# Performance work log

Measured on AMD Instinct MI355X. Metric: run time of the kernel, lower is better.

## Reference

```python
import jax, jax.numpy as jnp
import numpy as np

STRIDE = 16
SIZES = np.array([128.0, 256.0, 512.0], np.float32)
RATIOS = np.array([0.5, 1.0, 2.0], np.float32)
N_POS, N_NEG = 32, 32          # n_sample=64, pos_ratio=0.5
POS_THR, NEG_THR = 0.7, 0.2
W_CONF, W_REG = 1.0, 5.0


def _conv(x, w, b, stride, pad):
    y = jax.lax.conv_general_dilated(x, w, (stride, stride), [(pad, pad), (pad, pad)],
                                     dimension_numbers=('NCHW', 'OIHW', 'NCHW'))
    return y + b[None, :, None, None]


def _anchors(fw, fh, stride):
    # 9 anchors per center: 3 sizes x 3 aspect ratios
    ws = (SIZES[:, None] * np.sqrt(RATIOS)[None, :]).reshape(-1)
    hs = (SIZES[:, None] / np.sqrt(RATIOS)[None, :]).reshape(-1)
    wh = jnp.asarray(np.stack([ws, hs], -1))                      # (9,2)
    cx = (jnp.arange(fw, dtype=jnp.float32) + 0.5) * stride
    cy = (jnp.arange(fh, dtype=jnp.float32) + 0.5) * stride
    gx, gy = jnp.meshgrid(cx, cy, indexing='ij')                  # x-major, like the torch list comp
    ctr = jnp.stack([gx, gy], -1)[:, :, None, :]                  # (fw,fh,1,2)
    tl = ctr - wh / 2.0
    xywh = jnp.concatenate([tl, jnp.broadcast_to(wh, tl.shape)], -1)  # (fw,fh,9,4)
    return xywh.reshape(-1, 4)


def _xywh_to_xyxy(b):
    return jnp.concatenate([b[:, :2], b[:, :2] + b[:, 2:]], -1)


def _iou(a, b):  # a [N,4], b [M,4], xyxy
    lt = jnp.maximum(a[:, None, :2], b[None, :, :2])
    rb = jnp.minimum(a[:, None, 2:], b[None, :, 2:])
    inter = jnp.clip(rb - lt, 0.0).prod(-1)
    aa = (a[:, 2] - a[:, 0]) * (a[:, 3] - a[:, 1])
    ab = (b[:, 2] - b[:, 0]) * (b[:, 3] - b[:, 1])
    return inter / (aa[:, None] + ab[None, :] - inter)


def _head_flat(y, per):  # [1, 9*per, H, W] -> [W*H*9, per], matching anchor flatten order
    _, _, H, W = y.shape
    return y[0].reshape(9, per, H, W).transpose(3, 2, 0, 1).reshape(-1, per)


def _apply_offsets(boxes, off):  # decode proposals from xyxy boxes + (dx,dy,dw,dh)
    w = boxes[:, 2] - boxes[:, 0]; h = boxes[:, 3] - boxes[:, 1]
    cx = boxes[:, 0] + 0.5 * w;    cy = boxes[:, 1] + 0.5 * h
    ncx = cx + off[:, 0] * w;      ncy = cy + off[:, 1] * h
    nw = w * jnp.exp(off[:, 2]);   nh = h * jnp.exp(off[:, 3])
    return jnp.stack([ncx - nw / 2, ncy - nh / 2, ncx + nw / 2, ncy + nh / 2], -1)


def _box_offset(anc, gt):
    aw = anc[:, 2] - anc[:, 0]; ah = anc[:, 3] - anc[:, 1]
    acx = anc[:, 0] + 0.5 * aw; acy = anc[:, 1] + 0.5 * ah
    gw = gt[:, 2] - gt[:, 0];   gh = gt[:, 3] - gt[:, 1]
    gcx = gt[:, 0] + 0.5 * gw;  gcy = gt[:, 1] + 0.5 * gh
    return jnp.stack([(gcx - acx) / aw, (gcy - acy) / ah,
                      jnp.log(gw / aw), jnp.log(gh / ah)], -1)


def setup_inputs():
    key = jax.random.key(0)
    ks = jax.random.split(key, 12)
    img_data = jax.random.normal(ks[0], (1, 3, 1600, 1600), jnp.float32)
    x1 = jax.random.uniform(ks[1], (64,), minval=0.0, maxval=1400.0)
    y1 = jax.random.uniform(ks[2], (64,), minval=0.0, maxval=1400.0)
    bw = jax.random.uniform(ks[3], (64,), minval=32.0, maxval=200.0)
    bh = jax.random.uniform(ks[4], (64,), minval=32.0, maxval=200.0)
    gt_boxes = jnp.stack([x1, y1, x1 + bw, y1 + bh], -1)[None]   # [1,64,4], all valid (no -1 pad)
    gt_classes = jax.random.randint(ks[5], (1, 64), 1, 21, jnp.int32)
    def w(k, shape, fan):
        return jax.random.normal(k, shape, jnp.float32) * np.float32(np.sqrt(2.0 / fan))
    return dict(
        img_data=img_data, gt_boxes=gt_boxes, gt_classes=gt_classes,
        w1=w(ks[6], (64, 3, 7, 7), 3 * 49),      b1=jnp.zeros(64, jnp.float32),
        w2=w(ks[7], (256, 64, 3, 3), 64 * 9),    b2=jnp.zeros(256, jnp.float32),
        w_rpn=w(ks[8], (256, 256, 3, 3), 256 * 9), b_rpn=jnp.zeros(256, jnp.float32),
        w_cls=w(ks[9], (18, 256, 1, 1), 256),    b_cls=jnp.zeros(18, jnp.float32),
        w_reg=w(ks[10], (36, 256, 1, 1), 256),   b_reg=jnp.zeros(36, jnp.float32),
    )


def reference(img_data, gt_boxes, gt_classes, w1, b1, w2, b2, w_rpn, b_rpn, w_cls, b_cls, w_reg, b_reg):
    # --- feature extractor (total stride 16) ---
    fm = jax.nn.relu(_conv(img_data, w1, b1, 4, 3))
    fm = jax.nn.relu(_conv(fm, w2, b2, 4, 1))            # [1,256,100,100]
    H, W = fm.shape[2], fm.shape[3]
    # --- anchors + IoU matching ---
    anchors_xywh = _anchors(W, H, STRIDE)                # [N,4] xywh
    anchors_xyxy = _xywh_to_xyxy(anchors_xywh)
    gt = gt_boxes[0]                                     # [M,4], all valid
    ious = _iou(anchors_xyxy, gt)                        # [N,M]
    N = ious.shape[0]
    gt_max = ious.max(0)                                 # best iou per gt
    is_gt_best = (ious == gt_max[None, :]).any(1)        # torch: where(iou == gt_max)[0]
    anc_argmax = ious.argmax(1)
    anc_max = ious.max(1)
    labels = jnp.full((N,), -1.0, jnp.float32)
    labels = jnp.where(anc_max < NEG_THR, 0.0, labels)
    labels = jnp.where(is_gt_best, 1.0, labels)
    labels = jnp.where(anc_max > POS_THR, 1.0, labels)
    # --- deterministic pos/neg sampling (fixed sizes; replaces randperm subsampling) ---
    idx = jnp.arange(N, dtype=jnp.float32)
    _, pos_index = jax.lax.top_k(jnp.where(labels == 1.0, anc_max, -1.0), N_POS)
    _, neg_index = jax.lax.top_k(jnp.where(labels == 0.0, 1e6 - idx, -1e9), N_NEG)
    bboxes_pos = anchors_xyxy[pos_index]                 # box_convert(xywh->xyxy) of pos anchors
    # --- proposal module (RPN head) ---
    h = jax.nn.relu(_conv(fm, w_rpn, b_rpn, 1, 1))
    cls = _head_flat(_conv(h, w_cls, b_cls, 1, 0), 2)    # [N,2]
    reg = _head_flat(_conv(h, w_reg, b_reg, 1, 0), 4)    # [N,4]
    pos_score = cls[pos_index]
    neg_score = cls[neg_index]
    offset_pos = reg[pos_index]
    proposals = _apply_offsets(bboxes_pos, offset_pos)
    # --- losses ---
    gt_offset = _box_offset(bboxes_pos, gt[anc_argmax[pos_index]])
    logits = jnp.concatenate([pos_score, neg_score], 0)  # [64,2]
    tgt = jnp.concatenate([jnp.ones(N_POS, jnp.int32), jnp.zeros(N_NEG, jnp.int32)])
    logp = jax.nn.log_softmax(logits, -1)
    cls_loss = -logp[jnp.arange(N_POS + N_NEG), tgt].mean()
    d = gt_offset - offset_pos
    ad = jnp.abs(d)
    reg_loss = jnp.where(ad < 1.0, 0.5 * d * d, ad - 0.5).mean()
    total_rpn_loss = W_CONF * cls_loss + W_REG * reg_loss
    gt_cls_pos = gt_classes[0][anc_argmax[pos_index]]
    return (total_rpn_loss, fm, proposals, pos_index, gt_cls_pos)
```

## Files before the change

kernel.cpp:

```cpp
#include <hip/hip_runtime.h>
#include <math.h>


#define CAP 4096

typedef __attribute__((ext_vector_type(8))) short bf16x8;
typedef __attribute__((ext_vector_type(4))) float f32x4;

#define OFF_F1T     0
#define OFF_HBUF    0
#define OFF_FMT     5171328
#define OFF_CPART   6503040
#define OFF_RPART   7223040
#define OFF_WA1     8663040
#define OFF_W9_2    8672448
#define OFF_W9_3    8746176
#define OFF_WTC     9041088
#define OFF_WTG     9045696
#define OFF_AARG    9054912
#define OFF_NEGM    9144912
#define OFF_POSM    9147728
#define OFF_GTMAX   9150544
#define OFF_PIDX    9150624
#define OFF_NIDX    9150656
#define OFF_CANDS   9150688
#define OFF_CANDI   9154784

__device__ __forceinline__ unsigned short f2bf(float f) {
    unsigned int u = __float_as_uint(f);
    u += 0x7fffu + ((u >> 16) & 1u);
    return (unsigned short)(u >> 16);
}

__device__ __forceinline__ void anchor_box(int i, float& x0, float& y0,
                                           float& x1, float& y1, float& area) {
#pragma clang fp contract(off)
    const float sizes[3]  = {128.f, 256.f, 512.f};
    const float ratios[3] = {0.5f, 1.f, 2.f};
    int a = i % 9;
    int q = i / 9;
    int iy = q % 100;
    int ix = q / 100;
    int s = a / 3, r = a % 3;
    float sq = sqrtf(ratios[r]);
    float w = sizes[s] * sq;
    float h = sizes[s] / sq;
    float cx = ((float)ix + 0.5f) * 16.0f;
    float cy = ((float)iy + 0.5f) * 16.0f;
    x0 = cx - w * 0.5f;
    y0 = cy - h * 0.5f;
    x1 = x0 + w;
    y1 = y0 + h;
    area = (x1 - x0) * (y1 - y0);
}

__device__ __forceinline__ float iou_one(float ax0, float ay0, float ax1, float ay1, float aa,
                                         float bx0, float by0, float bx1, float by1, float ab) {
#pragma clang fp contract(off)
    float ltx = fmaxf(ax0, bx0), lty = fmaxf(ay0, by0);
    float rbx = fminf(ax1, bx1), rby = fminf(ay1, by1);
    float iw = fmaxf(rbx - ltx, 0.0f);
    float ih = fmaxf(rby - lty, 0.0f);
    float inter = iw * ih;
    return inter / ((aa + ab) - inter);
}

__global__ __launch_bounds__(256) void setup_kernel(const float* __restrict__ wc, float* __restrict__ wtc,
                                                    const float* __restrict__ wg, float* __restrict__ wtg,
                                                    const float* __restrict__ w1, unsigned short* __restrict__ wa1,
                                                    const float* __restrict__ w2, unsigned short* __restrict__ w9_2,
                                                    const float* __restrict__ wr, unsigned short* __restrict__ w9_3,
                                                    unsigned int* __restrict__ f1t_u, unsigned int* __restrict__ fmt_u,
                                                    unsigned int* __restrict__ gtmax) {
    int i = blockIdx.x * 256 + threadIdx.x;
    if (i < 65) { gtmax[i] = 0u; return; }
    i -= 65;
    if (i < 103040) {
        if (i < 51328) {
            int p = i >> 5, part = i & 31;
            int x, y;
            if (p < 804) { y = (p < 402) ? 0 : 401; x = p % 402; }
            else { int j = p - 804; x = (j < 400) ? 0 : 401; y = 1 + (j % 400); }
            f1t_u[(y * 402 + x) * 32 + part] = 0u;
        } else {
            int i2 = i - 51328;
            int p = i2 >> 7, part = i2 & 127;
            int x, y;
            if (p < 204) { y = (p < 102) ? 0 : 101; x = p % 102; }
            else { int j = p - 204; x = (j < 100) ? 0 : 101; y = 1 + (j % 100); }
            fmt_u[(y * 102 + x) * 128 + part] = 0u;
        }
        return;
    }
    i -= 103040;
    if (i < 4608) { int c = i / 256, k = i - c * 256; wtc[k * 18 + c] = wc[i]; return; }
    i -= 4608;
    if (i < 9216) { int c = i / 256, k = i - c * 256; wtg[k * 36 + c] = wg[i]; return; }
    i -= 9216;
    if (i < 10240) {
        int oc = i / 160, k = i - oc * 160;
        wa1[i] = (k < 147) ? f2bf(w1[oc * 147 + k]) : (unsigned short)0;
        return;
    }
    i -= 10240;
    if (i < 147456) {
        int kk = i / 16384; int rem = i - kk * 16384;
        int oc = rem / 64, ic = rem - oc * 64;
        w9_2[i] = f2bf(w2[(oc * 64 + ic) * 9 + kk]);
        return;
    }
    i -= 147456;
    if (i < 589824) {
        int cc = i / 16384; int rem = i - cc * 16384;
        int oc = rem / 64, icl = rem - oc * 64;
        int kk = cc / 4, ch = cc - kk * 4;
        w9_3[i] = f2bf(wr[(oc * 256 + ch * 64 + icl) * 9 + kk]);
    }
}

__global__ __launch_bounds__(256) void conv1_mfma(const float* __restrict__ img,
                                                  const unsigned short* __restrict__ wA,
                                                  const float* __restrict__ bias,
                                                  unsigned short* __restrict__ f1t) {
    __shared__ float sin_[3 * 7 * 260];
    __shared__ unsigned short tileT[64 * 72];
    int t = threadIdx.x;
    int wave = t >> 6, lane = t & 63;
    int quad = lane >> 4, l16 = lane & 15;
    int oy = blockIdx.y;
    int ox0 = blockIdx.x * 64;
    int gx0 = ox0 * 4 - 3;
    int gy0 = 4 * oy - 3;
    for (int idx = t; idx < 3 * 7 * 259; idx += 256) {
        int ic = idx / (7 * 259);
        int r = idx - ic * 7 * 259;
        int ky = r / 259, c = r - ky * 259;
        int gy = gy0 + ky, gx = gx0 + c;
        float v = 0.f;
        if (gy >= 0 && gy < 1600 && gx >= 0 && gx < 1600)
            v = img[(ic * 1600 + gy) * 1600 + gx];
        sin_[(ic * 7 + ky) * 260 + c] = v;
    }
    bf16x8 afr[5];
    {
        const bf16x8* ap = (const bf16x8*)(wA + (wave * 16 + l16) * 160 + quad * 8);
#pragma unroll
        for (int c = 0; c < 5; c++) afr[c] = ap[c * 4];
    }
    __syncthreads();

    f32x4 acc[4];
#pragma unroll
    for (int j = 0; j < 4; j++) acc[j] = (f32x4){0.f, 0.f, 0.f, 0.f};
    int q8 = quad * 8;
    int col4[4];
#pragma unroll
    for (int j = 0; j < 4; j++) col4[j] = 4 * (j * 16 + l16);

#pragma unroll
    for (int ch = 0; ch < 5; ch++) {
        float val[4][8];
#pragma unroll
        for (int jj = 0; jj < 8; jj++) {
            int k = ch * 32 + q8 + jj;
            int ic = (k * 335) >> 14;
            int r = k - ic * 49;
            int ky = (r * 37) >> 8;
            int kx = r - ky * 7;
            bool valid = (k < 147);
            int base = valid ? ((ic * 7 + ky) * 260 + kx) : 0;
#pragma unroll
            for (int j = 0; j < 4; j++) {
                float v = sin_[base + col4[j]];
                val[j][jj] = valid ? v : 0.f;
            }
        }
#pragma unroll
        for (int j = 0; j < 4; j++) {
            bf16x8 b;
#pragma unroll
            for (int jj = 0; jj < 8; jj++) b[jj] = (short)f2bf(val[j][jj]);
            acc[j] = __builtin_amdgcn_mfma_f32_16x16x32_bf16(afr[ch], b, acc[j], 0, 0, 0);
        }
    }
#pragma unroll
    for (int reg = 0; reg < 4; reg++) {
        int oc = wave * 16 + quad * 4 + reg;
        float bv = bias[oc];
#pragma unroll
        for (int j = 0; j < 4; j++) {
            int px = j * 16 + l16;
            tileT[px * 72 + oc] = f2bf(fmaxf(acc[j][reg] + bv, 0.f));
        }
    }
    __syncthreads();
    int px = t >> 2, part = t & 3;
    int ox = ox0 + px;
    if (ox < 400) {
        int row = (oy + 1) * 402 + ox + 1;
        uint4 v = *(const uint4*)(tileT + px * 72 + part * 16);
        *(uint4*)(f1t + row * 64 + part * 16) = v;
    }
}

template<int ICC, int RS, int S, bool WRT>
__global__ __launch_bounds__(256, 2) void conv_gemm(const unsigned short* __restrict__ Bt,
                                                    const unsigned short* __restrict__ A9,
                                                    const float* __restrict__ bias,
                                                    float* __restrict__ outF,
                                                    unsigned short* __restrict__ outT) {
    const int NC = ICC / 64;
    const int HC = S * 24 + 3;
    const int LROW = ICC + 8;
    __shared__ unsigned short blds[3 * HC * LROW];
    __shared__ unsigned short alds[256 * 72];
    int t = threadIdx.x;
    int xs = blockIdx.x, y = blockIdx.y;

    const int CHW = ICC / 8;
    for (int idx = t; idx < 3 * HC * CHW; idx += 256) {
        int row = idx / CHW, e = idx - row * CHW;
        int ky = row / HC, c = row - ky * HC;
        const uint4* src = (const uint4*)(Bt + ((size_t)(S * y + ky) * RS + S * xs * 25 + c) * ICC) + e;
        *(uint4*)(blds + row * LROW + e * 8) = *src;
    }
    int wave = t >> 6, lane = t & 63;
    int quad = lane >> 4, l16 = lane & 15;
    int oc0 = wave * 64;
    int pxe0 = min(l16, 24);
    int pxe1 = min(16 + l16, 24);

    f32x4 acc[4][2];
#pragma unroll
    for (int mt = 0; mt < 4; mt++)
#pragma unroll
        for (int j = 0; j < 2; j++) acc[mt][j] = (f32x4){0.f, 0.f, 0.f, 0.f};

    const unsigned short* a0 = alds + (oc0 + l16) * 72 + quad * 8;
    for (int cc = 0; cc < 9 * NC; cc++) {
        int pass = cc / NC, ch = cc - pass * NC;
        int ky = pass / 3, kx = pass - (pass / 3) * 3;
        __syncthreads();
        const uint4* asrc = (const uint4*)(A9 + (size_t)cc * 16384);
#pragma unroll
        for (int i = 0; i < 8; i++) {
            int e = i * 256 + t;
            *(uint4*)(alds + (e >> 3) * 72 + (e & 7) * 8) = asrc[e];
        }
        __syncthreads();
        const unsigned short* b0 = blds + (ky * HC + S * pxe0 + kx) * LROW + ch * 64 + quad * 8;
        const unsigned short* b1 = blds + (ky * HC + S * pxe1 + kx) * LROW + ch * 64 + quad * 8;
#pragma unroll
        for (int kcl = 0; kcl < 2; kcl++) {
            bf16x8 bf0 = *(const bf16x8*)(b0 + kcl * 32);
            bf16x8 bf1 = *(const bf16x8*)(b1 + kcl * 32);
#pragma unroll
            for (int mt = 0; mt < 4; mt++) {
                bf16x8 af = *(const bf16x8*)(a0 + mt * 16 * 72 + kcl * 32);
                acc[mt][0] = __builtin_amdgcn_mfma_f32_16x16x32_bf16(af, bf0, acc[mt][0], 0, 0, 0);
                acc[mt][1] = __builtin_amdgcn_mfma_f32_16x16x32_bf16(af, bf1, acc[mt][1], 0, 0, 0);
            }
        }
    }
#pragma unroll
    for (int mt = 0; mt < 4; mt++) {
#pragma unroll
        for (int reg = 0; reg < 4; reg++) {
            int oc = oc0 + mt * 16 + quad * 4 + reg;
            float bv = bias[oc];
#pragma unroll
            for (int j = 0; j < 2; j++) {
                int pl = j * 16 + l16;
                if (pl < 25) {
                    int p = y * 100 + xs * 25 + pl;
                    float v = fmaxf(acc[mt][j][reg] + bv, 0.f);
                    outF[oc * 10000 + p] = v;
                    if (WRT) {
                        int r = (y + 1) * 102 + xs * 25 + pl + 1;
                        outT[r * 256 + oc] = f2bf(v);
                    }
                }
            }
        }
    }
}

__global__ __launch_bounds__(64) void head_kernel(const float* __restrict__ hbuf,
                                                  const float* __restrict__ wtc,
                                                  const float* __restrict__ wtg,
                                                  float* __restrict__ cpart,
                                                  float* __restrict__ rpart) {
    int p = blockIdx.x * 64 + threadIdx.x;
    int ch = blockIdx.y;
    int ic0 = ch * 64;
    if (p >= 10000) return;
    float acc[54];
#pragma unroll
    for (int j = 0; j < 54; j++) acc[j] = 0.f;
    for (int ic = 0; ic < 64; ic++) {
        float v = hbuf[(ic0 + ic) * 10000 + p];
        const float* wc_ = wtc + (ic0 + ic) * 18;
#pragma unroll
        for (int j = 0; j < 18; j++) acc[j] += v * wc_[j];
        const float* wg_ = wtg + (ic0 + ic) * 36;
#pragma unroll
        for (int j = 0; j < 36; j++) acc[18 + j] += v * wg_[j];
    }
    for (int j = 0; j < 18; j++) cpart[(ch * 18 + j) * 10000 + p] = acc[j];
    for (int j = 0; j < 36; j++) rpart[(ch * 36 + j) * 10000 + p] = acc[18 + j];
}

__global__ __launch_bounds__(256) void iou_pass1(const float* __restrict__ gt,
                                                 int* __restrict__ aarg,
                                                 unsigned int* __restrict__ gtmax) {
    __shared__ float sg[64][4];
    __shared__ float sarea[64];
    __shared__ unsigned int smax[64];
    int t = threadIdx.x;
    if (t < 64) {
#pragma clang fp contract(off)
        float b0 = gt[t * 4 + 0], b1 = gt[t * 4 + 1];
        float b2 = gt[t * 4 + 2], b3 = gt[t * 4 + 3];
        sg[t][0] = b0; sg[t][1] = b1; sg[t][2] = b2; sg[t][3] = b3;
        sarea[t] = (b2 - b0) * (b3 - b1);
        smax[t] = 0u;
    }
    __syncthreads();
    int i = blockIdx.x * 256 + t;
    int iq = min(i, 89999);
    float x0, y0, x1, y1, aa;
    anchor_box(iq, x0, y0, x1, y1, aa);
    float best = -1.f;
    int bestj = 0;
    for (int j = 0; j < 64; j++) {
        float v = iou_one(x0, y0, x1, y1, aa, sg[j][0], sg[j][1], sg[j][2], sg[j][3], sarea[j]);
        if (v > best) { best = v; bestj = j; }
        float vm = v;
#pragma unroll
        for (int off = 32; off > 0; off >>= 1) vm = fmaxf(vm, __shfl_xor(vm, off));
        if ((t & 63) == 0) atomicMax(&smax[j], __float_as_uint(vm));
    }
    if (i < 90000) aarg[i] = bestj;
    __syncthreads();
    if (t < 64) atomicMax(&gtmax[t], smax[t]);
}

__global__ __launch_bounds__(256) void iou_pass2(const float* __restrict__ gt,
                                                 const unsigned int* __restrict__ gtmax,
                                                 unsigned long long* __restrict__ negmask,
                                                 unsigned long long* __restrict__ posmask,
                                                 float* __restrict__ cand_s,
                                                 int* __restrict__ cand_i,
                                                 unsigned int* __restrict__ cnt) {
    __shared__ float sg[64][4];
    __shared__ float sarea[64];
    __shared__ float sgm[64];
    int t = threadIdx.x;
    if (t < 64) {
#pragma clang fp contract(off)
        float b0 = gt[t * 4 + 0], b1 = gt[t * 4 + 1];
        float b2 = gt[t * 4 + 2], b3 = gt[t * 4 + 3];
        sg[t][0] = b0; sg[t][1] = b1; sg[t][2] = b2; sg[t][3] = b3;
        sarea[t] = (b2 - b0) * (b3 - b1);
        sgm[t] = __uint_as_float(gtmax[t]);
    }
    __syncthreads();
    int i = blockIdx.x * 256 + t;
    if (i >= 90000) return;
    float x0, y0, x1, y1, aa;
    anchor_box(i, x0, y0, x1, y1, aa);
    float best = -1.f;
    bool isbest = false;
    for (int j = 0; j < 64; j++) {
        float v = iou_one(x0, y0, x1, y1, aa, sg[j][0], sg[j][1], sg[j][2], sg[j][3], sarea[j]);
        if (v > best) best = v;
        if (v == sgm[j]) isbest = true;
    }
    float label = -1.f;
    if (best < 0.2f) label = 0.f;
    if (isbest) label = 1.f;
    if (best > 0.7f) label = 1.f;
    unsigned long long negb = __ballot(label == 0.f);
    unsigned long long posb = __ballot(label == 1.f);
    if ((t & 63) == 0) { negmask[i >> 6] = negb; posmask[i >> 6] = posb; }
    if (label == 1.f) {
        unsigned int p = atomicAdd(cnt, 1u);
        if (p < CAP) { cand_s[p] = best; cand_i[p] = i; }
    }
}

__device__ int first32_from_mask(const unsigned long long* __restrict__ mask,
                                 bool invert, int* __restrict__ outIdx,
                                 int* scnt, int t) {
    const int NW = 1407;
    const int WPT = 6;
    unsigned long long mw[WPT];
    int cnt = 0;
#pragma unroll
    for (int u = 0; u < WPT; u++) {
        int w = t * WPT + u;
        unsigned long long m = 0ull;
        if (w < NW) {
            m = mask[w];
            if (invert) m = ~m;
            if (w == NW - 1) m &= 0xFFFFull;
        }
        mw[u] = m;
        cnt += __builtin_popcountll(m);
    }
    scnt[t] = cnt;
    __syncthreads();
    for (int off = 1; off < 256; off <<= 1) {
        int v = (t >= off) ? scnt[t - off] : 0;
        __syncthreads();
        scnt[t] += v;
        __syncthreads();
    }
    int total = scnt[255];
    int pref = scnt[t] - cnt;
    if (pref < 32) {
#pragma unroll
        for (int u = 0; u < WPT; u++) {
            unsigned long long m = mw[u];
            int wbase = (t * WPT + u) * 64;
            while (m && pref < 32) {
                int b = __builtin_ctzll(m);
                outIdx[pref++] = wbase + b;
                m &= m - 1;
            }
        }
    }
    __syncthreads();
    return total;
}

__global__ __launch_bounds__(256) void select_kernel(const unsigned long long* __restrict__ negmask,
                                                     const unsigned long long* __restrict__ posmask,
                                                     const float* __restrict__ cand_s,
                                                     const int* __restrict__ cand_i,
                                                     const unsigned int* __restrict__ cnt,
                                                     int* __restrict__ pidx,
                                                     int* __restrict__ nidx) {
    __shared__ float cs[CAP + 32];
    __shared__ int ci[CAP + 32];
    __shared__ int scnt[256];
    __shared__ int sfill[32];
    __shared__ float rs[256];
    __shared__ int ri[256];
    __shared__ int rslot[256];
    int t = threadIdx.x;
    int ncand = min((int)*cnt, CAP);
    for (int c = t; c < ncand; c += 256) { cs[c] = cand_s[c]; ci[c] = cand_i[c]; }
    __syncthreads();

    int nfill = 0;
    if (ncand < 32) {
        int tot = first32_from_mask(posmask, true, sfill, scnt, t);
        nfill = min(tot, 32);
        for (int k = t; k < nfill; k += 256) { cs[ncand + k] = -1.0f; ci[ncand + k] = sfill[k]; }
    }
    __syncthreads();
    int ntot = ncand + nfill;

    for (int s = 0; s < 32; s++) {
        float bs = -1e30f;
        int bi = 0x7fffffff;
        int bsl = -1;
        for (int c = t; c < ntot; c += 256) {
            float v = cs[c];
            int id = ci[c];
            if (v > bs || (v == bs && id < bi)) { bs = v; bi = id; bsl = c; }
        }
        rs[t] = bs; ri[t] = bi; rslot[t] = bsl;
        __syncthreads();
        for (int off = 128; off > 0; off >>= 1) {
            if (t < off) {
                if (rs[t + off] > rs[t] || (rs[t + off] == rs[t] && ri[t + off] < ri[t])) {
                    rs[t] = rs[t + off]; ri[t] = ri[t + off]; rslot[t] = rslot[t + off];
                }
            }
            __syncthreads();
        }
        if (t == 0) { pidx[s] = ri[0]; cs[rslot[0]] = -1e30f; }
        __syncthreads();
    }

    int totn = first32_from_mask(negmask, false, nidx, scnt, t);
    if (t == 0) {
        int nf = min(totn, 32);
        for (int s = nf; s < 32; s++) nidx[s] = s;
    }
}

__global__ __launch_bounds__(64) void finalize_kernel(const float* __restrict__ cpart,
                                                      const float* __restrict__ rpart,
                                                      const float* __restrict__ bcls,
                                                      const float* __restrict__ breg,
                                                      const int* __restrict__ pidx,
                                                      const int* __restrict__ nidx,
                                                      const int* __restrict__ aarg,
                                                      const float* __restrict__ gt,
                                                      const int* __restrict__ gtc,
                                                      float* __restrict__ out) {
#pragma clang fp contract(off)
    const int PROP_OFF = 1 + 2560000;
    int t = threadIdx.x;
    int n = (t < 32) ? pidx[t] : nidx[t - 32];
    int a = n % 9;
    int q = n / 9;
    int iy = q % 100;
    int ix = q / 100;
    int p = iy * 100 + ix;

    float l0 = bcls[a * 2 + 0], l1 = bcls[a * 2 + 1];
    for (int c = 0; c < 4; c++) {
        l0 += cpart[(c * 18 + a * 2 + 0) * 10000 + p];
        l1 += cpart[(c * 18 + a * 2 + 1) * 10000 + p];
    }
    float m = fmaxf(l0, l1);
    float lse = m + logf(expf(l0 - m) + expf(l1 - m));
    float logp = ((t < 32) ? l1 : l0) - lse;
    float cls_sum = logp;
#pragma unroll
    for (int off = 32; off > 0; off >>= 1) cls_sum += __shfl_down(cls_sum, off);

    float reg_sum = 0.f;
    if (t < 32) {
        float offv[4];
#pragma unroll
        for (int k = 0; k < 4; k++) {
            float v = breg[a * 4 + k];
            for (int c = 0; c < 4; c++) v += rpart[(c * 36 + a * 4 + k) * 10000 + p];
            offv[k] = v;
        }
        float x0, y0, x1, y1, aa;
        anchor_box(n, x0, y0, x1, y1, aa);
        float w = x1 - x0, h = y1 - y0;
        float cx = x0 + 0.5f * w, cy = y0 + 0.5f * h;
        float ncx = cx + offv[0] * w, ncy = cy + offv[1] * h;
        float nw = w * expf(offv[2]), nh = h * expf(offv[3]);
        out[PROP_OFF + t * 4 + 0] = ncx - nw * 0.5f;
        out[PROP_OFF + t * 4 + 1] = ncy - nh * 0.5f;
        out[PROP_OFF + t * 4 + 2] = ncx + nw * 0.5f;
        out[PROP_OFF + t * 4 + 3] = ncy + nh * 0.5f;

        int j = aarg[n];
        float g0 = gt[j * 4 + 0], g1 = gt[j * 4 + 1];
        float g2 = gt[j * 4 + 2], g3 = gt[j * 4 + 3];
        float gw = g2 - g0, gh = g3 - g1;
        float gcx = g0 + 0.5f * gw, gcy = g1 + 0.5f * gh;
        float tg[4];
        tg[0] = (gcx - cx) / w;
        tg[1] = (gcy - cy) / h;
        tg[2] = logf(gw / w);
        tg[3] = logf(gh / h);
#pragma unroll
        for (int k = 0; k < 4; k++) {
            float d = tg[k] - offv[k];
            float ad = fabsf(d);
            reg_sum += (ad < 1.f) ? 0.5f * d * d : ad - 0.5f;
        }
        out[PROP_OFF + 128 + t] = (float)n;
        out[PROP_OFF + 160 + t] = (float)gtc[j];
    }
#pragma unroll
    for (int off = 32; off > 0; off >>= 1) reg_sum += __shfl_down(reg_sum, off);
    if (t == 0) {
        float cls_loss = -(cls_sum / 64.f);
        float reg_loss = reg_sum / 128.f;
        out[0] = cls_loss + 5.f * reg_loss;
    }
}

extern "C" void kernel_launch(void* const* d_in, const int* in_sizes, int n_in,
                              void* d_out, int out_size, void* d_ws, size_t ws_size,
                              hipStream_t stream) {
    const float* img = (const float*)d_in[0];
    const float* gt  = (const float*)d_in[1];
    const int*   gtc = (const int*)d_in[2];
    const float* w1  = (const float*)d_in[3];
    const float* b1  = (const float*)d_in[4];
    const float* w2  = (const float*)d_in[5];
    const float* b2  = (const float*)d_in[6];
    const float* wr  = (const float*)d_in[7];
    const float* br  = (const float*)d_in[8];
    const float* wc  = (const float*)d_in[9];
    const float* bc  = (const float*)d_in[10];
    const float* wg  = (const float*)d_in[11];
    const float* bg  = (const float*)d_in[12];
    float* out = (float*)d_out;
    float* ws = (float*)d_ws;

    unsigned short* f1t  = (unsigned short*)(ws + OFF_F1T);
    unsigned short* fmt  = (unsigned short*)(ws + OFF_FMT);
    unsigned short* wa1  = (unsigned short*)(ws + OFF_WA1);
    unsigned short* w9_2 = (unsigned short*)(ws + OFF_W9_2);
    unsigned short* w9_3 = (unsigned short*)(ws + OFF_W9_3);
    float* hbuf  = ws + OFF_HBUF;
    float* cpart = ws + OFF_CPART;
    float* rpart = ws + OFF_RPART;
    float* wtc   = ws + OFF_WTC;
    float* wtg   = ws + OFF_WTG;
    int*   aarg  = (int*)(ws + OFF_AARG);
    unsigned long long* negm = (unsigned long long*)(ws + OFF_NEGM);
    unsigned long long* posm = (unsigned long long*)(ws + OFF_POSM);
    unsigned int* gtmax = (unsigned int*)(ws + OFF_GTMAX);
    unsigned int* cnt   = gtmax + 64;
    int*   pidx  = (int*)(ws + OFF_PIDX);
    int*   nidx  = (int*)(ws + OFF_NIDX);
    float* cands = ws + OFF_CANDS;
    int*   candi = (int*)(ws + OFF_CANDI);
    float* fm    = out + 1;

    setup_kernel<<<dim3(3377), dim3(256), 0, stream>>>(wc, wtc, wg, wtg, w1, wa1,
                                                       w2, w9_2, wr, w9_3,
                                                       (unsigned int*)f1t, (unsigned int*)fmt, gtmax);

    conv1_mfma<<<dim3(7, 400), dim3(256), 0, stream>>>(img, wa1, b1, f1t);
    conv_gemm<64, 402, 4, true><<<dim3(4, 100), dim3(256), 0, stream>>>(f1t, w9_2, b2, fm, fmt);
    conv_gemm<256, 102, 1, false><<<dim3(4, 100), dim3(256), 0, stream>>>(fmt, w9_3, br, hbuf, nullptr);
    head_kernel<<<dim3(157, 4), dim3(64), 0, stream>>>(hbuf, wtc, wtg, cpart, rpart);

    iou_pass1<<<dim3(352), dim3(256), 0, stream>>>(gt, aarg, gtmax);
    iou_pass2<<<dim3(352), dim3(256), 0, stream>>>(gt, gtmax, negm, posm, cands, candi, cnt);
    select_kernel<<<dim3(1), dim3(256), 0, stream>>>(negm, posm, cands, candi, cnt, pidx, nidx);
    finalize_kernel<<<dim3(1), dim3(64), 0, stream>>>(cpart, rpart, bc, bg, pidx, nidx,
                                                      aarg, gt, gtc, out);
}
```

Before: 325.3 us.

## Fuse select and finalize into single-wave tail kernel with packed-key top-k

Merges the selection and finalize kernels into one 64-thread kernel, which removes a launch and the global round trip for the selected indices. Score and index are packed into one 64-bit sortable key. The 32 top-k rounds use wave shuffles instead of shared-memory reductions with barriers, and only the lane that held the winner rescans its slice. The mask prefix scan also becomes a wave shuffle scan with 22 words per lane. The cost is that the whole tail now runs on a single wave, so the candidate scan is less parallel when there are many candidates.

Result: faster. 299.9 us (-7.8%).

```diff
diff --git a/kernel.cpp b/kernel.cpp
--- a/kernel.cpp
+++ b/kernel.cpp
@@ -21,8 +21,6 @@
 #define OFF_NEGM    9144912
 #define OFF_POSM    9147728
 #define OFF_GTMAX   9150544
-#define OFF_PIDX    9150624
-#define OFF_NIDX    9150656
 #define OFF_CANDS   9150688
 #define OFF_CANDI   9154784
 
@@ -389,16 +387,21 @@
     }
 }
 
-__device__ int first32_from_mask(const unsigned long long* __restrict__ mask,
-                                 bool invert, int* __restrict__ outIdx,
-                                 int* scnt, int t) {
+__device__ __forceinline__ unsigned long long shflx64(unsigned long long v, int m) {
+    int lo = __shfl_xor((int)(unsigned)(v & 0xFFFFFFFFull), m);
+    int hi = __shfl_xor((int)(unsigned)(v >> 32), m);
+    return ((unsigned long long)(unsigned)hi << 32) | (unsigned)lo;
+}
+
+__device__ int wave_first32(const unsigned long long* __restrict__ mask,
+                            bool invert, int* __restrict__ outIdx, int lane) {
     const int NW = 1407;
-    const int WPT = 6;
+    const int WPT = 22;
     unsigned long long mw[WPT];
     int cnt = 0;
 #pragma unroll
     for (int u = 0; u < WPT; u++) {
-        int w = t * WPT + u;
+        int w = lane * WPT + u;
         unsigned long long m = 0ull;
         if (w < NW) {
             m = mask[w];
@@ -408,21 +411,19 @@
         mw[u] = m;
         cnt += __builtin_popcountll(m);
     }
-    scnt[t] = cnt;
-    __syncthreads();
-    for (int off = 1; off < 256; off <<= 1) {
-        int v = (t >= off) ? scnt[t - off] : 0;
-        __syncthreads();
-        scnt[t] += v;
-        __syncthreads();
-    }
-    int total = scnt[255];
-    int pref = scnt[t] - cnt;
+    int inc = cnt;
+#pragma unroll
+    for (int off = 1; off < 64; off <<= 1) {
+        int v = __shfl_up(inc, off);
+        if (lane >= off) inc += v;
+    }
+    int total = __shfl(inc, 63);
+    int pref = inc - cnt;
     if (pref < 32) {
 #pragma unroll
         for (int u = 0; u < WPT; u++) {
             unsigned long long m = mw[u];
-            int wbase = (t * WPT + u) * 64;
+            int wbase = (lane * WPT + u) * 64;
             while (m && pref < 32) {
                 int b = __builtin_ctzll(m);
                 outIdx[pref++] = wbase + b;
@@ -430,145 +431,142 @@
             }
         }
     }
-    __syncthreads();
     return total;
 }
 
-__global__ __launch_bounds__(256) void select_kernel(const unsigned long long* __restrict__ negmask,
-                                                     const unsigned long long* __restrict__ posmask,
-                                                     const float* __restrict__ cand_s,
-                                                     const int* __restrict__ cand_i,
-                                                     const unsigned int* __restrict__ cnt,
-                                                     int* __restrict__ pidx,
-                                                     int* __restrict__ nidx) {
-    __shared__ float cs[CAP + 32];
-    __shared__ int ci[CAP + 32];
-    __shared__ int scnt[256];
+__global__ __launch_bounds__(64) void tail_kernel(const unsigned long long* __restrict__ negmask,
+                                                  const unsigned long long* __restrict__ posmask,
+                                                  const float* __restrict__ cand_s,
+                                                  const int* __restrict__ cand_i,
+                                                  const unsigned int* __restrict__ cnt,
+                                                  const float* __restrict__ cpart,
+                                                  const float* __restrict__ rpart,
+                                                  const float* __restrict__ bcls,
+                                                  const float* __restrict__ breg,
+                                                  const int* __restrict__ aarg,
+                                                  const float* __restrict__ gt,
+                                                  const int* __restrict__ gtc,
+                                                  float* __restrict__ out) {
+    __shared__ unsigned long long keys[CAP + 32];
     __shared__ int sfill[32];
-    __shared__ float rs[256];
-    __shared__ int ri[256];
-    __shared__ int rslot[256];
-    int t = threadIdx.x;
+    __shared__ int spidx[32];
+    __shared__ int snidx[32];
+    int lane = threadIdx.x;
+
     int ncand = min((int)*cnt, CAP);
-    for (int c = t; c < ncand; c += 256) { cs[c] = cand_s[c]; ci[c] = cand_i[c]; }
-    __syncthreads();
-
-    int nfill = 0;
+    for (int c = lane; c < ncand; c += 64) {
+        unsigned u = __float_as_uint(cand_s[c]);
+        u ^= (u & 0x80000000u) ? 0xFFFFFFFFu : 0x80000000u;
+        keys[c] = ((unsigned long long)u << 32) | (0xFFFFFFFFu - (unsigned)cand_i[c]);
+    }
+    int ntot = ncand;
     if (ncand < 32) {
-        int tot = first32_from_mask(posmask, true, sfill, scnt, t);
-        nfill = min(tot, 32);
-        for (int k = t; k < nfill; k += 256) { cs[ncand + k] = -1.0f; ci[ncand + k] = sfill[k]; }
-    }
-    __syncthreads();
-    int ntot = ncand + nfill;
-
+        int tot = wave_first32(posmask, true, sfill, lane);
+        int nfill = min(tot, 32);
+        unsigned um1 = __float_as_uint(-1.0f) ^ 0xFFFFFFFFu;
+        for (int k2 = lane; k2 < nfill; k2 += 64)
+            keys[ncand + k2] = ((unsigned long long)um1 << 32) | (0xFFFFFFFFu - (unsigned)sfill[k2]);
+        ntot += nfill;
+    }
+
+    unsigned long long lk = 0ull; int ls = -1;
+    for (int c = lane; c < ntot; c += 64) {
+        unsigned long long k = keys[c];
+        if (k > lk) { lk = k; ls = c; }
+    }
     for (int s = 0; s < 32; s++) {
-        float bs = -1e30f;
-        int bi = 0x7fffffff;
-        int bsl = -1;
-        for (int c = t; c < ntot; c += 256) {
-            float v = cs[c];
-            int id = ci[c];
-            if (v > bs || (v == bs && id < bi)) { bs = v; bi = id; bsl = c; }
-        }
-        rs[t] = bs; ri[t] = bi; rslot[t] = bsl;
-        __syncthreads();
-        for (int off = 128; off > 0; off >>= 1) {
-            if (t < off) {
-                if (rs[t + off] > rs[t] || (rs[t + off] == rs[t] && ri[t + off] < ri[t])) {
-                    rs[t] = rs[t + off]; ri[t] = ri[t + off]; rslot[t] = rslot[t + off];
-                }
+        unsigned long long mk = lk;
+#pragma unroll
+        for (int off = 1; off < 64; off <<= 1) {
+            unsigned long long o = shflx64(mk, off);
+            if (o > mk) mk = o;
+        }
+        if (lk == mk && mk != 0ull) {
+            spidx[s] = (int)(0xFFFFFFFFu - (unsigned)(mk & 0xFFFFFFFFull));
+            keys[ls] = 0ull;
+            lk = 0ull; ls = -1;
+            for (int c = lane; c < ntot; c += 64) {
+                unsigned long long k = keys[c];
+                if (k > lk) { lk = k; ls = c; }
             }
-            __syncthreads();
-        }
-        if (t == 0) { pidx[s] = ri[0]; cs[rslot[0]] = -1e30f; }
-        __syncthreads();
-    }
-
-    int totn = first32_from_mask(negmask, false, nidx, scnt, t);
-    if (t == 0) {
+        }
+    }
+
+    int totn = wave_first32(negmask, false, snidx, lane);
+    if (lane == 0) {
         int nf = min(totn, 32);
-        for (int s = nf; s < 32; s++) nidx[s] = s;
-    }
-}
-
-__global__ __launch_bounds__(64) void finalize_kernel(const float* __restrict__ cpart,
-                                                      const float* __restrict__ rpart,
-                                                      const float* __restrict__ bcls,
-                                                      const float* __restrict__ breg,
-                                                      const int* __restrict__ pidx,
-                                                      const int* __restrict__ nidx,
-                                                      const int* __restrict__ aarg,
-                                                      const float* __restrict__ gt,
-                                                      const int* __restrict__ gtc,
-                                                      float* __restrict__ out) {
+        for (int s = nf; s < 32; s++) snidx[s] = s;
+    }
+
+    {
 #pragma clang fp contract(off)
-    const int PROP_OFF = 1 + 2560000;
-    int t = threadIdx.x;
-    int n = (t < 32) ? pidx[t] : nidx[t - 32];
-    int a = n % 9;
-    int q = n / 9;
-    int iy = q % 100;
-    int ix = q / 100;
-    int p = iy * 100 + ix;
-
-    float l0 = bcls[a * 2 + 0], l1 = bcls[a * 2 + 1];
-    for (int c = 0; c < 4; c++) {
-        l0 += cpart[(c * 18 + a * 2 + 0) * 10000 + p];
-        l1 += cpart[(c * 18 + a * 2 + 1) * 10000 + p];
-    }
-    float m = fmaxf(l0, l1);
-    float lse = m + logf(expf(l0 - m) + expf(l1 - m));
-    float logp = ((t < 32) ? l1 : l0) - lse;
-    float cls_sum = logp;
-#pragma unroll
-    for (int off = 32; off > 0; off >>= 1) cls_sum += __shfl_down(cls_sum, off);
-
-    float reg_sum = 0.f;
-    if (t < 32) {
-        float offv[4];
-#pragma unroll
-        for (int k = 0; k < 4; k++) {
-            float v = breg[a * 4 + k];
-            for (int c = 0; c < 4; c++) v += rpart[(c * 36 + a * 4 + k) * 10000 + p];
-            offv[k] = v;
-        }
-        float x0, y0, x1, y1, aa;
-        anchor_box(n, x0, y0, x1, y1, aa);
-        float w = x1 - x0, h = y1 - y0;
-        float cx = x0 + 0.5f * w, cy = y0 + 0.5f * h;
-        float ncx = cx + offv[0] * w, ncy = cy + offv[1] * h;
-        float nw = w * expf(offv[2]), nh = h * expf(offv[3]);
-        out[PROP_OFF + t * 4 + 0] = ncx - nw * 0.5f;
-        out[PROP_OFF + t * 4 + 1] = ncy - nh * 0.5f;
-        out[PROP_OFF + t * 4 + 2] = ncx + nw * 0.5f;
-        out[PROP_OFF + t * 4 + 3] = ncy + nh * 0.5f;
-
-        int j = aarg[n];
-        float g0 = gt[j * 4 + 0], g1 = gt[j * 4 + 1];
-        float g2 = gt[j * 4 + 2], g3 = gt[j * 4 + 3];
-        float gw = g2 - g0, gh = g3 - g1;
-        float gcx = g0 + 0.5f * gw, gcy = g1 + 0.5f * gh;
-        float tg[4];
-        tg[0] = (gcx - cx) / w;
-        tg[1] = (gcy - cy) / h;
-        tg[2] = logf(gw / w);
-        tg[3] = logf(gh / h);
-#pragma unroll
-        for (int k = 0; k < 4; k++) {
-            float d = tg[k] - offv[k];
-            float ad = fabsf(d);
-            reg_sum += (ad < 1.f) ? 0.5f * d * d : ad - 0.5f;
-        }
-        out[PROP_OFF + 128 + t] = (float)n;
-        out[PROP_OFF + 160 + t] = (float)gtc[j];
-    }
-#pragma unroll
-    for (int off = 32; off > 0; off >>= 1) reg_sum += __shfl_down(reg_sum, off);
-    if (t == 0) {
-        float cls_loss = -(cls_sum / 64.f);
-        float reg_loss = reg_sum / 128.f;
-        out[0] = cls_loss + 5.f * reg_loss;
+        const int PROP_OFF = 1 + 2560000;
+        int t = lane;
+        int n = (t < 32) ? spidx[t] : snidx[t - 32];
+        int a = n % 9;
+        int q = n / 9;
+        int iy = q % 100;
+        int ix = q / 100;
+        int p = iy * 100 + ix;
+
+        float l0 = bcls[a * 2 + 0], l1 = bcls[a * 2 + 1];
+        for (int c = 0; c < 4; c++) {
+            l0 += cpart[(c * 18 + a * 2 + 0) * 10000 + p];
+            l1 += cpart[(c * 18 + a * 2 + 1) * 10000 + p];
+        }
+        float m = fmaxf(l0, l1);
+        float lse = m + logf(expf(l0 - m) + expf(l1 - m));
+        float logp = ((t < 32) ? l1 : l0) - lse;
+        float cls_sum = logp;
+#pragma unroll
+        for (int off = 32; off > 0; off >>= 1) cls_sum += __shfl_down(cls_sum, off);
+
+        float reg_sum = 0.f;
+        if (t < 32) {
+            float offv[4];
+#pragma unroll
+            for (int k = 0; k < 4; k++) {
+                float v = breg[a * 4 + k];
+                for (int c = 0; c < 4; c++) v += rpart[(c * 36 + a * 4 + k) * 10000 + p];
+                offv[k] = v;
+            }
+            float x0, y0, x1, y1, aa;
+            anchor_box(n, x0, y0, x1, y1, aa);
+            float w = x1 - x0, h = y1 - y0;
+            float cx = x0 + 0.5f * w, cy = y0 + 0.5f * h;
+            float ncx = cx + offv[0] * w, ncy = cy + offv[1] * h;
+            float nw = w * expf(offv[2]), nh = h * expf(offv[3]);
+            out[PROP_OFF + t * 4 + 0] = ncx - nw * 0.5f;
+            out[PROP_OFF + t * 4 + 1] = ncy - nh * 0.5f;
+            out[PROP_OFF + t * 4 + 2] = ncx + nw * 0.5f;
+            out[PROP_OFF + t * 4 + 3] = ncy + nh * 0.5f;
+
+            int j = aarg[n];
+            float g0 = gt[j * 4 + 0], g1 = gt[j * 4 + 1];
+            float g2 = gt[j * 4 + 2], g3 = gt[j * 4 + 3];
+            float gw = g2 - g0, gh = g3 - g1;
+            float gcx = g0 + 0.5f * gw, gcy = g1 + 0.5f * gh;
+            float tg[4];
+            tg[0] = (gcx - cx) / w;
+            tg[1] = (gcy - cy) / h;
+            tg[2] = logf(gw / w);
+            tg[3] = logf(gh / h);
+#pragma unroll
+            for (int k = 0; k < 4; k++) {
+                float d = tg[k] - offv[k];
+                float ad = fabsf(d);
+                reg_sum += (ad < 1.f) ? 0.5f * d * d : ad - 0.5f;
+            }
+            out[PROP_OFF + 128 + t] = (float)n;
+            out[PROP_OFF + 160 + t] = (float)gtc[j];
+        }
+#pragma unroll
+        for (int off = 32; off > 0; off >>= 1) reg_sum += __shfl_down(reg_sum, off);
+        if (t == 0) {
+            float cls_loss = -(cls_sum / 64.f);
+            float reg_loss = reg_sum / 128.f;
+            out[0] = cls_loss + 5.f * reg_loss;
+        }
     }
 }
 
@@ -606,8 +604,6 @@
     unsigned long long* posm = (unsigned long long*)(ws + OFF_POSM);
     unsigned int* gtmax = (unsigned int*)(ws + OFF_GTMAX);
     unsigned int* cnt   = gtmax + 64;
-    int*   pidx  = (int*)(ws + OFF_PIDX);
-    int*   nidx  = (int*)(ws + OFF_NIDX);
     float* cands = ws + OFF_CANDS;
     int*   candi = (int*)(ws + OFF_CANDI);
     float* fm    = out + 1;
@@ -623,7 +619,6 @@
 
     iou_pass1<<<dim3(352), dim3(256), 0, stream>>>(gt, aarg, gtmax);
     iou_pass2<<<dim3(352), dim3(256), 0, stream>>>(gt, gtmax, negm, posm, cands, candi, cnt);
-    select_kernel<<<dim3(1), dim3(256), 0, stream>>>(negm, posm, cands, candi, cnt, pidx, nidx);
-    finalize_kernel<<<dim3(1), dim3(64), 0, stream>>>(cpart, rpart, bc, bg, pidx, nidx,
-                                                      aarg, gt, gtc, out);
-}
+    tail_kernel<<<dim3(1), dim3(64), 0, stream>>>(negm, posm, cands, candi, cnt,
+                                                  cpart, rpart, bc, bg, aarg, gt, gtc, out);
+}
```
